# Optimization experiments

Hardware: AMD Instinct MI355X
Metric: run time of the kernel (lower is better)

The kernel has to match this reference:

```python
import jax, jax.numpy as jnp
import numpy as np

# dims
T, B, IN, OUT = 100, 128, 512, 512
# LIF constants (match torch defaults / init_kwargs)
TAU_TRACE, TAU_MEM, TAU_SYN, DT = 20.0, 20.0, 5.0, 1.0
THRESH, SSB = 1.0, 0.03


def setup_inputs() -> dict:
    key = jax.random.key(0)
    k1, k2 = jax.random.split(key)
    input_spikes = (jax.random.uniform(k1, (T, B, IN)) < 0.1).astype(jnp.float32)
    W = jax.random.normal(k2, (OUT, IN), dtype=jnp.float32) * (1.0 / IN ** 0.5)
    return {"input_spikes": input_spikes, "W": W}


def reference(input_spikes, W):
    alpha = jnp.exp(jnp.asarray(-DT / TAU_SYN, jnp.float32))   # synaptic decay
    beta = jnp.exp(jnp.asarray(-DT / TAU_MEM, jnp.float32))    # membrane decay
    gamma = jnp.exp(jnp.asarray(-DT / TAU_TRACE, jnp.float32)) # trace decay
    Tn, Bn, _ = input_spikes.shape
    out_f, in_f = W.shape
    I0 = jnp.zeros((Bn, out_f), jnp.float32)
    U0 = jnp.zeros((Bn, out_f), jnp.float32)
    tr0 = jnp.zeros((Bn, out_f, in_f), jnp.float32)

    def step(carry, x_t):
        I, U, trace = carry
        I = alpha * I + x_t @ W.T                      # (B, out)
        U = beta * U + I
        S = (U >= THRESH).astype(jnp.float32)
        U_pre = U                                      # first U_hist append (pre-reset)
        U = U - S * THRESH                             # reset
        du = jnp.abs(U - THRESH)
        sigma_prime = 1.0 / (1.0 + SSB * du) ** 2      # SuperSpike surrogate
        # eligibility trace: outer product of surrogate grad and input spikes
        trace = gamma * trace + sigma_prime[:, :, None] * x_t[:, None, :]
        U_post = U                                     # second U_hist append (post-reset)
        U = U - S * THRESH                             # second subtraction (as in source)
        return (I, U, trace), (S, U_pre, U_post)

    (_, _, trace), (S, U_pre, U_post) = jax.lax.scan(step, (I0, U0, tr0), input_spikes)
    # interleave pre/post membrane snapshots -> (2T, B, out), matching the torch stack order
    U_hist = jnp.stack([U_pre, U_post], axis=1).reshape(2 * Tn, Bn, out_f)
    return S, U_hist, trace
```

## Files before the change

kernel.cpp:

```cpp
#include <hip/hip_runtime.h>

#define T_STEPS 100
#define B_N     128
#define IN_F    512
#define OUT_F   512

#define ALPHA_D 0.8187307530779818
#define BETA_D  0.9512294245007140

typedef __attribute__((ext_vector_type(8))) short bf16x8;
typedef __attribute__((ext_vector_type(4))) float f32x4;

static __device__ __forceinline__ unsigned short f2bf(float f) {
    union { float f; unsigned int u; } v; v.f = f;
    unsigned int r = (v.u + 0x7FFFu + ((v.u >> 16) & 1u)) >> 16;
    return (unsigned short)r;
}

__global__ __launch_bounds__(256) void transposeW(const float* __restrict__ W,
                                                  float* __restrict__ Wt) {
    __shared__ float tile[32][33];
    const int bx = blockIdx.x & 15;
    const int by = blockIdx.x >> 4;
    const int tx = threadIdx.x & 31;
    const int ty = threadIdx.x >> 5;
#pragma unroll
    for (int k = 0; k < 32; k += 8) {
        int o = by * 32 + ty + k;
        tile[ty + k][tx] = W[o * IN_F + bx * 32 + tx];
    }
    __syncthreads();
#pragma unroll
    for (int k = 0; k < 32; k += 8) {
        int i = bx * 32 + ty + k;
        Wt[i * OUT_F + by * 32 + tx] = tile[tx][ty + k];
    }
}

__global__ __launch_bounds__(256) void syn_current(const float* __restrict__ x,
                                                   const float* __restrict__ Wt,
                                                   double* __restrict__ C) {
    const int tb  = blockIdx.x;
    const int tid = threadIdx.x;

    __shared__ int s_idx[IN_F];
    __shared__ int s_cnt;

    if (tid < 64) {
        const float* xr = x + (size_t)tb * IN_F;
        int base = 0;
#pragma unroll
        for (int j = 0; j < 8; ++j) {
            const float v = xr[j * 64 + tid];
            const unsigned long long m = __ballot(v > 0.5f);
            if (v > 0.5f) {
                const int pos = base + __popcll(m & ((1ull << tid) - 1ull));
                s_idx[pos] = j * 64 + tid;
            }
            base += __popcll(m);
        }
        if (tid == 0) s_cnt = base;
    }
    __syncthreads();

    const int cnt = s_cnt;
    double c0 = 0.0, c1 = 0.0;
    const float* W0 = Wt + tid;
    const float* W1 = Wt + tid + 256;
    for (int k = 0; k < cnt; ++k) {
        const int i = s_idx[k];
        c0 += (double)W0[(size_t)i * OUT_F];
        c1 += (double)W1[(size_t)i * OUT_F];
    }

    double* Cr = C + (size_t)tb * OUT_F;
    Cr[tid]       = c0;
    Cr[tid + 256] = c1;
}

#define LIF_STEP(BUF, J, CB)                                                   \
    {                                                                          \
        const int t = (CB) * 10 + (J);                                         \
        I = ALPHA_D * I + BUF[J];                                              \
        U = BETA_D * U + I;                                                    \
        const double Sv = (U >= 1.0) ? 1.0 : 0.0;                              \
        S_out[(size_t)t * N + pos] = (float)Sv;                                \
        Uh[(size_t)(2 * t) * N + pos] = (float)U;                              \
        U -= Sv;                                                               \
        Uh[(size_t)(2 * t + 1) * N + pos] = (float)U;                          \
        U -= Sv;                                                               \
    }

__global__ __launch_bounds__(256) void lif_pointwise(const double* __restrict__ C,
                                                     float* __restrict__ S_out,
                                                     float* __restrict__ Uh) {
    const int pos = blockIdx.x * 256 + threadIdx.x;
    const size_t N = (size_t)B_N * OUT_F;

    double I = 0.0, U = 0.0;
    double bufA[10], bufB[10];

#pragma unroll
    for (int j = 0; j < 10; ++j) bufA[j] = C[(size_t)j * N + pos];

    for (int cb = 0; cb < 10; cb += 2) {
#pragma unroll
        for (int j = 0; j < 10; ++j) bufB[j] = C[((size_t)(cb + 1) * 10 + j) * N + pos];
#pragma unroll
        for (int j = 0; j < 10; ++j) LIF_STEP(bufA, j, cb)
        if (cb + 2 < 10) {
#pragma unroll
            for (int j = 0; j < 10; ++j) bufA[j] = C[((size_t)(cb + 2) * 10 + j) * N + pos];
        }
#pragma unroll
        for (int j = 0; j < 10; ++j) LIF_STEP(bufB, j, cb + 1)
    }
}

__global__ __launch_bounds__(256) void trace_mfma(const float* __restrict__ x,
                                                  const float* __restrict__ Uh,
                                                  float* __restrict__ trace) {
    __shared__ unsigned short Pa[128 * 128];
    __shared__ unsigned short Xb[128 * 128];

    const int idx  = blockIdx.x;
    const int xcd  = idx & 7;
    const int slot = idx >> 3;
    const int b    = xcd * 16 + (slot >> 4);
    const int tile = slot & 15;
    const int ot   = tile >> 2;
    const int it   = tile & 3;
    const int tid  = threadIdx.x;

    char* const pbase = (char*)Pa;
    char* const xbase = (char*)Xb;

#pragma unroll
    for (int r = 0; r < 8; ++r) {
        const int g  = tid + r * 256;
        const int i  = g & 127;
        const int kg = g >> 7;
        unsigned int h[4];
#pragma unroll
        for (int jj = 0; jj < 4; ++jj) {
            const int t0 = kg * 8 + jj * 2, t1 = t0 + 1;
            float v0 = 0.f, v1 = 0.f;
            if (t0 < T_STEPS) v0 = x[(size_t)t0 * (B_N * IN_F) + b * IN_F + it * 128 + i];
            if (t1 < T_STEPS) v1 = x[(size_t)t1 * (B_N * IN_F) + b * IN_F + it * 128 + i];
            h[jj] = (unsigned int)f2bf(v0) | ((unsigned int)f2bf(v1) << 16);
        }
        unsigned int off = (unsigned int)(i * 256 + kg * 16) ^ ((unsigned int)(i & 7) << 4);
        *(uint4*)(xbase + off) = make_uint4(h[0], h[1], h[2], h[3]);
    }

#pragma unroll
    for (int r = 0; r < 8; ++r) {
        const int g  = tid + r * 256;
        const int o  = g & 127;
        const int kg = g >> 7;
        unsigned int h[4];
#pragma unroll
        for (int jj = 0; jj < 4; ++jj) {
            unsigned int hw[2];
#pragma unroll
            for (int e = 0; e < 2; ++e) {
                const int t = kg * 8 + jj * 2 + e;
                float p = 0.f;
                if (t < T_STEPS) {
                    const float u  = Uh[(size_t)(2 * t + 1) * (B_N * OUT_F) + b * OUT_F + ot * 128 + o];
                    const float du = fabsf(u - 1.0f);
                    const float d  = 1.0f + 0.03f * du;
                    const float gp = __expf(-0.05f * (float)(T_STEPS - 1 - t));
                    p = gp / (d * d);
                }
                hw[e] = f2bf(p);
            }
            h[jj] = hw[0] | (hw[1] << 16);
        }
        unsigned int off = (unsigned int)(o * 256 + kg * 16) ^ ((unsigned int)(o & 7) << 4);
        *(uint4*)(pbase + off) = make_uint4(h[0], h[1], h[2], h[3]);
    }
    __syncthreads();

    const int w    = tid >> 6;
    const int l    = tid & 63;
    const int wo   = (w >> 1) * 64;
    const int wi   = (w & 1) * 64;
    const int lo16 = l & 15;
    const int g4   = l >> 4;

    f32x4 acc[4][4];
#pragma unroll
    for (int m = 0; m < 4; ++m)
#pragma unroll
        for (int n = 0; n < 4; ++n) acc[m][n] = (f32x4){0.f, 0.f, 0.f, 0.f};

#pragma unroll
    for (int kk = 0; kk < 4; ++kk) {
        bf16x8 af[4], bfr[4];
#pragma unroll
        for (int m = 0; m < 4; ++m) {
            const int row = wo + m * 16 + lo16;
            const unsigned int off = (unsigned int)(row * 256 + kk * 64 + g4 * 16)
                                     ^ ((unsigned int)(row & 7) << 4);
            af[m] = *(const bf16x8*)(pbase + off);
        }
#pragma unroll
        for (int n = 0; n < 4; ++n) {
            const int row = wi + n * 16 + lo16;
            const unsigned int off = (unsigned int)(row * 256 + kk * 64 + g4 * 16)
                                     ^ ((unsigned int)(row & 7) << 4);
            bfr[n] = *(const bf16x8*)(xbase + off);
        }
#pragma unroll
        for (int m = 0; m < 4; ++m)
#pragma unroll
            for (int n = 0; n < 4; ++n)
                acc[m][n] = __builtin_amdgcn_mfma_f32_16x16x32_bf16(af[m], bfr[n], acc[m][n], 0, 0, 0);
    }

    float* tb = trace + (size_t)b * (OUT_F * IN_F);
#pragma unroll
    for (int m = 0; m < 4; ++m) {
#pragma unroll
        for (int rr = 0; rr < 4; ++rr) {
            const int o = ot * 128 + wo + m * 16 + g4 * 4 + rr;
#pragma unroll
            for (int n = 0; n < 4; ++n) {
                const int i = it * 128 + wi + n * 16 + lo16;
                tb[(size_t)o * IN_F + i] = acc[m][n][rr];
            }
        }
    }
}

extern "C" void kernel_launch(void* const* d_in, const int* in_sizes, int n_in,
                              void* d_out, int out_size, void* d_ws, size_t ws_size,
                              hipStream_t stream) {
    const float* x = (const float*)d_in[0];
    const float* W = (const float*)d_in[1];

    float* out   = (float*)d_out;
    float* S_out = out;
    float* Uh    = out + (size_t)T_STEPS * B_N * OUT_F;
    float* trace = Uh + (size_t)2 * T_STEPS * B_N * OUT_F;

    float* Wt = (float*)d_ws;

    double* C = (double*)trace;

    transposeW<<<256, 256, 0, stream>>>(W, Wt);
    syn_current<<<T_STEPS * B_N, 256, 0, stream>>>(x, Wt, C);
    lif_pointwise<<<B_N * OUT_F / 256, 256, 0, stream>>>(C, S_out, Uh);
    trace_mfma<<<16 * B_N, 256, 0, stream>>>(x, Uh, trace);
}
```

Before: 158.1 us.

## Precompute bf16 surrogate and input operands in workspace for trace MFMA

Adds a kernel that converts the input spikes to a padded bf16 K-major layout, and has the LIF kernel emit the decay-weighted surrogate gradient directly as packed bf16. The trace MFMA kernel then loads both operands with contiguous 16-byte vector loads instead of gathering strided fp32 values and converting them per tile. This removes redundant conversion and scattered loads across the 16 tiles per batch. In exchange it adds an extra kernel launch, extra workspace traffic and per-step exp/division work in the LIF kernel. It falls back to the old path when the workspace is too small.

```diff
diff --git a/kernel.cpp b/kernel.cpp
--- a/kernel.cpp
+++ b/kernel.cpp
@@ -4,6 +4,7 @@
 #define B_N     128
 #define IN_F    512
 #define OUT_F   512
+#define KPAD    128
 
 #define ALPHA_D 0.8187307530779818
 #define BETA_D  0.9512294245007140
@@ -11,10 +12,9 @@
 typedef __attribute__((ext_vector_type(8))) short bf16x8;
 typedef __attribute__((ext_vector_type(4))) float f32x4;
 
-static __device__ __forceinline__ unsigned short f2bf(float f) {
+static __device__ __forceinline__ unsigned int f2bf(float f) {
     union { float f; unsigned int u; } v; v.f = f;
-    unsigned int r = (v.u + 0x7FFFu + ((v.u >> 16) & 1u)) >> 16;
-    return (unsigned short)r;
+    return (v.u + 0x7FFFu + ((v.u >> 16) & 1u)) >> 16;
 }
 
 __global__ __launch_bounds__(256) void transposeW(const float* __restrict__ W,
@@ -34,6 +34,31 @@
     for (int k = 0; k < 32; k += 8) {
         int i = bx * 32 + ty + k;
         Wt[i * OUT_F + by * 32 + tx] = tile[tx][ty + k];
+    }
+}
+
+__global__ __launch_bounds__(256) void x_to_bf16(const float* __restrict__ x,
+                                                 unsigned short* __restrict__ Xbf) {
+    const int b   = blockIdx.x & (B_N - 1);
+    const int i0  = (blockIdx.x >> 7) * 128;
+    const int tid = threadIdx.x;
+
+#pragma unroll
+    for (int r = 0; r < 8; ++r) {
+        const int g = tid + r * 256;
+        const int i = i0 + (g & 127);
+        const int c = g >> 7;
+        unsigned int h[4];
+#pragma unroll
+        for (int jj = 0; jj < 4; ++jj) {
+            const int t0 = c * 8 + jj * 2, t1 = t0 + 1;
+            float v0 = 0.f, v1 = 0.f;
+            if (t0 < T_STEPS) v0 = x[(size_t)t0 * (B_N * IN_F) + b * IN_F + i];
+            if (t1 < T_STEPS) v1 = x[(size_t)t1 * (B_N * IN_F) + b * IN_F + i];
+            h[jj] = f2bf(v0) | (f2bf(v1) << 16);
+        }
+        *(uint4*)((char*)Xbf + (size_t)(b * IN_F + i) * (KPAD * 2) + c * 16) =
+            make_uint4(h[0], h[1], h[2], h[3]);
     }
 }
 
@@ -88,17 +113,27 @@
         Uh[(size_t)(2 * t) * N + pos] = (float)U;                              \
         U -= Sv;                                                               \
         Uh[(size_t)(2 * t + 1) * N + pos] = (float)U;                          \
+        if (Pq) {                                                              \
+            const float du = fabsf((float)U - 1.0f);                           \
+            const float dd = 1.0f + 0.03f * du;                                \
+            const float pv = __expf(-0.05f * (float)(T_STEPS - 1 - t)) / (dd * dd); \
+            const unsigned int hw = f2bf(pv);                                  \
+            if ((J) & 1) Pq[(size_t)pos * 64 + (t >> 1)] = plo | (hw << 16);   \
+            else plo = hw;                                                     \
+        }                                                                      \
         U -= Sv;                                                               \
     }
 
 __global__ __launch_bounds__(256) void lif_pointwise(const double* __restrict__ C,
                                                      float* __restrict__ S_out,
-                                                     float* __restrict__ Uh) {
+                                                     float* __restrict__ Uh,
+                                                     unsigned int* __restrict__ Pq) {
     const int pos = blockIdx.x * 256 + threadIdx.x;
     const size_t N = (size_t)B_N * OUT_F;
 
     double I = 0.0, U = 0.0;
     double bufA[10], bufB[10];
+    unsigned int plo = 0;
 
 #pragma unroll
     for (int j = 0; j < 10; ++j) bufA[j] = C[(size_t)j * N + pos];
@@ -115,11 +150,16 @@
 #pragma unroll
         for (int j = 0; j < 10; ++j) LIF_STEP(bufB, j, cb + 1)
     }
-}
-
-__global__ __launch_bounds__(256) void trace_mfma(const float* __restrict__ x,
-                                                  const float* __restrict__ Uh,
-                                                  float* __restrict__ trace) {
+
+    if (Pq) {
+#pragma unroll
+        for (int k = 0; k < 14; ++k) Pq[(size_t)pos * 64 + 50 + k] = 0u;
+    }
+}
+
+__global__ __launch_bounds__(256) void trace_mfma_pre(const unsigned short* __restrict__ Pbf,
+                                                      const unsigned short* __restrict__ Xbf,
+                                                      float* __restrict__ trace) {
     __shared__ unsigned short Pa[128 * 128];
     __shared__ unsigned short Xb[128 * 128];
 
@@ -134,6 +174,91 @@
 
     char* const pbase = (char*)Pa;
     char* const xbase = (char*)Xb;
+    const char* const Pg = (const char*)Pbf + (size_t)(b * OUT_F + ot * 128) * (KPAD * 2);
+    const char* const Xg = (const char*)Xbf + (size_t)(b * IN_F + it * 128) * (KPAD * 2);
+
+#pragma unroll
+    for (int r = 0; r < 8; ++r) {
+        const int chunk = tid + r * 256;
+        const int row   = chunk >> 4;
+        const int c     = chunk & 15;
+        const unsigned int loff = (unsigned int)(row * 256) + ((unsigned int)(c * 16) ^ ((unsigned int)(row & 7) << 4));
+        const uint4 vp = *(const uint4*)(Pg + (size_t)row * 256 + c * 16);
+        const uint4 vx = *(const uint4*)(Xg + (size_t)row * 256 + c * 16);
+        *(uint4*)(pbase + loff) = vp;
+        *(uint4*)(xbase + loff) = vx;
+    }
+    __syncthreads();
+
+    const int w    = tid >> 6;
+    const int l    = tid & 63;
+    const int wo   = (w >> 1) * 64;
+    const int wi   = (w & 1) * 64;
+    const int lo16 = l & 15;
+    const int g4   = l >> 4;
+
+    f32x4 acc[4][4];
+#pragma unroll
+    for (int m = 0; m < 4; ++m)
+#pragma unroll
+        for (int n = 0; n < 4; ++n) acc[m][n] = (f32x4){0.f, 0.f, 0.f, 0.f};
+
+#pragma unroll
+    for (int kk = 0; kk < 4; ++kk) {
+        bf16x8 af[4], bfr[4];
+#pragma unroll
+        for (int m = 0; m < 4; ++m) {
+            const int row = wo + m * 16 + lo16;
+            const unsigned int off = (unsigned int)(row * 256 + kk * 64 + g4 * 16)
+                                     ^ ((unsigned int)(row & 7) << 4);
+            af[m] = *(const bf16x8*)(pbase + off);
+        }
+#pragma unroll
+        for (int n = 0; n < 4; ++n) {
+            const int row = wi + n * 16 + lo16;
+            const unsigned int off = (unsigned int)(row * 256 + kk * 64 + g4 * 16)
+                                     ^ ((unsigned int)(row & 7) << 4);
+            bfr[n] = *(const bf16x8*)(xbase + off);
+        }
+#pragma unroll
+        for (int m = 0; m < 4; ++m)
+#pragma unroll
+            for (int n = 0; n < 4; ++n)
+                acc[m][n] = __builtin_amdgcn_mfma_f32_16x16x32_bf16(af[m], bfr[n], acc[m][n], 0, 0, 0);
+    }
+
+    float* tb = trace + (size_t)b * (OUT_F * IN_F);
+#pragma unroll
+    for (int m = 0; m < 4; ++m) {
+#pragma unroll
+        for (int rr = 0; rr < 4; ++rr) {
+            const int o = ot * 128 + wo + m * 16 + g4 * 4 + rr;
+#pragma unroll
+            for (int n = 0; n < 4; ++n) {
+                const int i = it * 128 + wi + n * 16 + lo16;
+                tb[(size_t)o * IN_F + i] = acc[m][n][rr];
+            }
+        }
+    }
+}
+
+__global__ __launch_bounds__(256) void trace_mfma(const float* __restrict__ x,
+                                                  const float* __restrict__ Uh,
+                                                  float* __restrict__ trace) {
+    __shared__ unsigned short Pa[128 * 128];
+    __shared__ unsigned short Xb[128 * 128];
+
+    const int idx  = blockIdx.x;
+    const int xcd  = idx & 7;
+    const int slot = idx >> 3;
+    const int b    = xcd * 16 + (slot >> 4);
+    const int tile = slot & 15;
+    const int ot   = tile >> 2;
+    const int it   = tile & 3;
+    const int tid  = threadIdx.x;
+
+    char* const pbase = (char*)Pa;
+    char* const xbase = (char*)Xb;
 
 #pragma unroll
     for (int r = 0; r < 8; ++r) {
@@ -147,7 +272,7 @@
             float v0 = 0.f, v1 = 0.f;
             if (t0 < T_STEPS) v0 = x[(size_t)t0 * (B_N * IN_F) + b * IN_F + it * 128 + i];
             if (t1 < T_STEPS) v1 = x[(size_t)t1 * (B_N * IN_F) + b * IN_F + it * 128 + i];
-            h[jj] = (unsigned int)f2bf(v0) | ((unsigned int)f2bf(v1) << 16);
+            h[jj] = f2bf(v0) | (f2bf(v1) << 16);
         }
         unsigned int off = (unsigned int)(i * 256 + kg * 16) ^ ((unsigned int)(i & 7) << 4);
         *(uint4*)(xbase + off) = make_uint4(h[0], h[1], h[2], h[3]);
@@ -245,12 +370,23 @@
     float* Uh    = out + (size_t)T_STEPS * B_N * OUT_F;
     float* trace = Uh + (size_t)2 * T_STEPS * B_N * OUT_F;
 
-    float* Wt = (float*)d_ws;
+    const size_t WT_BYTES = (size_t)IN_F * OUT_F * 4;
+    const size_t BF_BYTES = (size_t)B_N * 512 * KPAD * 2;
+    const bool   ws_ok    = ws_size >= WT_BYTES + 2 * BF_BYTES;
+
+    float*          Wt  = (float*)d_ws;
+    unsigned short* Xbf = (unsigned short*)((char*)d_ws + WT_BYTES);
+    unsigned short* Pbf = (unsigned short*)((char*)d_ws + WT_BYTES + BF_BYTES);
 
     double* C = (double*)trace;
 
     transposeW<<<256, 256, 0, stream>>>(W, Wt);
+    if (ws_ok) x_to_bf16<<<512, 256, 0, stream>>>(x, Xbf);
     syn_current<<<T_STEPS * B_N, 256, 0, stream>>>(x, Wt, C);
-    lif_pointwise<<<B_N * OUT_F / 256, 256, 0, stream>>>(C, S_out, Uh);
-    trace_mfma<<<16 * B_N, 256, 0, stream>>>(x, Uh, trace);
-}
+    lif_pointwise<<<B_N * OUT_F / 256, 256, 0, stream>>>(C, S_out, Uh,
+                                                         ws_ok ? (unsigned int*)Pbf : nullptr);
+    if (ws_ok)
+        trace_mfma_pre<<<16 * B_N, 256, 0, stream>>>(Pbf, Xbf, trace);
+    else
+        trace_mfma<<<16 * B_N, 256, 0, stream>>>(x, Uh, trace);
+}
```

Result: slower. 165.3 us (+4.6%).

## Fuse synaptic current, LIF recurrence and trace MFMA into one kernel

Applied to the files above, without the earlier changes.

Replaces the three-kernel pipeline (syn_current, lif_pointwise, trace_mfma) with a spike-index prep kernel plus one fused kernel per (batch, 256-output) block. That kernel computes the sparse current, runs the LIF recurrence and keeps the surrogate weights in LDS for the trace matmul. This avoids the double-precision current buffer round trip and the re-read of Uh. The catch is that only 256 blocks are launched, each running a serial 100-step recurrence followed by a long trace phase, so occupancy is low. It also needs extra workspace and keeps the old path as a fallback.

```diff
diff --git a/kernel.cpp b/kernel.cpp
--- a/kernel.cpp
+++ b/kernel.cpp
@@ -11,10 +11,9 @@
 typedef __attribute__((ext_vector_type(8))) short bf16x8;
 typedef __attribute__((ext_vector_type(4))) float f32x4;
 
-static __device__ __forceinline__ unsigned short f2bf(float f) {
+static __device__ __forceinline__ unsigned int f2bf(float f) {
     union { float f; unsigned int u; } v; v.f = f;
-    unsigned int r = (v.u + 0x7FFFu + ((v.u >> 16) & 1u)) >> 16;
-    return (unsigned short)r;
+    return (v.u + 0x7FFFu + ((v.u >> 16) & 1u)) >> 16;
 }
 
 __global__ __launch_bounds__(256) void transposeW(const float* __restrict__ W,
@@ -34,6 +33,181 @@
     for (int k = 0; k < 32; k += 8) {
         int i = bx * 32 + ty + k;
         Wt[i * OUT_F + by * 32 + tx] = tile[tx][ty + k];
+    }
+}
+
+__global__ __launch_bounds__(256) void prep_lists(const float* __restrict__ x,
+                                                  unsigned char* __restrict__ Lg,
+                                                  int* __restrict__ Cg) {
+    const int pair = blockIdx.x * 4 + (threadIdx.x >> 6);
+    const int lane = threadIdx.x & 63;
+    const int t = pair >> 7, b = pair & 127;
+    const float* xr = x + (size_t)pair * IN_F;
+    unsigned char* lrow = Lg + (size_t)b * (128 * 128) + t * 128;
+    int base = 0, clo = 0;
+#pragma unroll
+    for (int j = 0; j < 8; ++j) {
+        const float v = xr[j * 64 + lane];
+        const unsigned long long m = __ballot(v > 0.5f);
+        if (v > 0.5f) {
+            const int pos = base + __popcll(m & ((1ull << lane) - 1ull));
+            lrow[pos] = (unsigned char)((j * 64 + lane) & 255);
+        }
+        base += __popcll(m);
+        if (j == 3) clo = base;
+    }
+    if (lane == 0) Cg[b * 128 + t] = clo | (base << 16);
+}
+
+__global__ __launch_bounds__(256) void fused_lif_trace(const float* __restrict__ x,
+                                                       const float* __restrict__ Wt,
+                                                       const unsigned char* __restrict__ Lg,
+                                                       const int* __restrict__ Cg,
+                                                       float* __restrict__ S_out,
+                                                       float* __restrict__ Uh,
+                                                       float* __restrict__ trace) {
+    __shared__ char smem[98816];
+    char* const Psm = smem;
+    char* const Lsm = smem + 65536;
+    int*  const Csm = (int*)(smem + 81920);
+    char* const Xsm = smem + 82432;
+
+    const int tid = threadIdx.x;
+    const int b   = blockIdx.x & 127;
+    const int ob  = blockIdx.x >> 7;
+
+    {
+        const uint4 z = make_uint4(0u, 0u, 0u, 0u);
+#pragma unroll
+        for (int r = 0; r < 16; ++r) ((uint4*)Psm)[tid + r * 256] = z;
+        const uint4* Lg4 = (const uint4*)(Lg + (size_t)b * (128 * 128));
+#pragma unroll
+        for (int r = 0; r < 4; ++r) ((uint4*)Lsm)[tid + r * 256] = Lg4[tid + r * 256];
+        if (tid < 128) Csm[tid] = Cg[b * 128 + tid];
+    }
+    __syncthreads();
+
+    {
+        const int og = ob * 256 + tid;
+        const float* const Wlo = Wt + og;
+        const float* const Whi = Wt + (size_t)256 * OUT_F + og;
+        const size_t N = (size_t)B_N * OUT_F;
+        const size_t base = (size_t)b * OUT_F + og;
+        double I = 0.0, U = 0.0;
+        for (int t = 0; t < T_STEPS; ++t) {
+            const int cp   = Csm[t];
+            const int clo  = cp & 0xFFFF;
+            const int ctot = cp >> 16;
+            const unsigned char* lp = (const unsigned char*)Lsm + t * 128;
+
+            double c0 = 0.0, c1 = 0.0, c2 = 0.0, c3 = 0.0;
+            int k = 0;
+            for (; k + 3 < clo; k += 4) {
+                c0 += (double)Wlo[(size_t)lp[k]     * OUT_F];
+                c1 += (double)Wlo[(size_t)lp[k + 1] * OUT_F];
+                c2 += (double)Wlo[(size_t)lp[k + 2] * OUT_F];
+                c3 += (double)Wlo[(size_t)lp[k + 3] * OUT_F];
+            }
+            for (; k < clo; ++k) c0 += (double)Wlo[(size_t)lp[k] * OUT_F];
+            for (; k + 3 < ctot; k += 4) {
+                c0 += (double)Whi[(size_t)lp[k]     * OUT_F];
+                c1 += (double)Whi[(size_t)lp[k + 1] * OUT_F];
+                c2 += (double)Whi[(size_t)lp[k + 2] * OUT_F];
+                c3 += (double)Whi[(size_t)lp[k + 3] * OUT_F];
+            }
+            for (; k < ctot; ++k) c0 += (double)Whi[(size_t)lp[k] * OUT_F];
+            const double c = (c0 + c2) + (c1 + c3);
+
+            I = ALPHA_D * I + c;
+            U = BETA_D * U + I;
+            const double Sv = (U >= 1.0) ? 1.0 : 0.0;
+            __builtin_nontemporal_store((float)Sv, S_out + (size_t)t * N + base);
+            __builtin_nontemporal_store((float)U,  Uh + (size_t)(2 * t) * N + base);
+            U -= Sv;
+            __builtin_nontemporal_store((float)U,  Uh + (size_t)(2 * t + 1) * N + base);
+            {
+                const float du = fabsf((float)U - 1.0f);
+                const float dd = 1.0f + 0.03f * du;
+                const float pv = __expf(-0.05f * (float)(T_STEPS - 1 - t)) / (dd * dd);
+                *(unsigned short*)(Psm + (((unsigned)(tid * 256 + 2 * t)) ^
+                                          (((unsigned)(tid & 7)) << 4))) = (unsigned short)f2bf(pv);
+            }
+            U -= Sv;
+        }
+    }
+    __syncthreads();
+
+    const int w = tid >> 6, l = tid & 63, lo16 = l & 15, g4 = l >> 4;
+
+    bf16x8 af[4][4];
+#pragma unroll
+    for (int m = 0; m < 4; ++m) {
+        const int row = w * 64 + m * 16 + lo16;
+#pragma unroll
+        for (int kk = 0; kk < 4; ++kk) {
+            const unsigned off = (unsigned)(row * 256 + kk * 64 + g4 * 16)
+                                 ^ ((unsigned)(row & 7) << 4);
+            af[m][kk] = *(const bf16x8*)(Psm + off);
+        }
+    }
+
+    float* const tb = trace + (size_t)b * (OUT_F * IN_F);
+
+    for (int it = 0; it < 8; ++it) {
+#pragma unroll
+        for (int r = 0; r < 4; ++r) {
+            const int g  = tid + r * 256;
+            const int i  = g & 63;
+            const int kg = g >> 6;
+            unsigned int h[4];
+#pragma unroll
+            for (int jj = 0; jj < 4; ++jj) {
+                const int t0 = kg * 8 + jj * 2, t1 = t0 + 1;
+                float v0 = 0.f, v1 = 0.f;
+                if (t0 < T_STEPS) v0 = x[(size_t)t0 * (B_N * IN_F) + b * IN_F + it * 64 + i];
+                if (t1 < T_STEPS) v1 = x[(size_t)t1 * (B_N * IN_F) + b * IN_F + it * 64 + i];
+                h[jj] = f2bf(v0) | (f2bf(v1) << 16);
+            }
+            const unsigned loff = (unsigned)(i * 256) +
+                (((unsigned)(kg * 16)) ^ (((unsigned)(i & 7)) << 4));
+            *(uint4*)(Xsm + loff) = make_uint4(h[0], h[1], h[2], h[3]);
+        }
+        __syncthreads();
+
+        f32x4 acc[4][4];
+#pragma unroll
+        for (int m = 0; m < 4; ++m)
+#pragma unroll
+            for (int n = 0; n < 4; ++n) acc[m][n] = (f32x4){0.f, 0.f, 0.f, 0.f};
+
+#pragma unroll
+        for (int kk = 0; kk < 4; ++kk) {
+            bf16x8 bfr[4];
+#pragma unroll
+            for (int n = 0; n < 4; ++n) {
+                const int row = n * 16 + lo16;
+                const unsigned off = (unsigned)(row * 256 + kk * 64 + g4 * 16)
+                                     ^ ((unsigned)(row & 7) << 4);
+                bfr[n] = *(const bf16x8*)(Xsm + off);
+            }
+#pragma unroll
+            for (int m = 0; m < 4; ++m)
+#pragma unroll
+                for (int n = 0; n < 4; ++n)
+                    acc[m][n] = __builtin_amdgcn_mfma_f32_16x16x32_bf16(af[m][kk], bfr[n], acc[m][n], 0, 0, 0);
+        }
+
+#pragma unroll
+        for (int m = 0; m < 4; ++m)
+#pragma unroll
+            for (int rr = 0; rr < 4; ++rr) {
+                const int o = ob * 256 + w * 64 + m * 16 + g4 * 4 + rr;
+#pragma unroll
+                for (int n = 0; n < 4; ++n)
+                    __builtin_nontemporal_store(acc[m][n][rr],
+                        tb + (size_t)o * IN_F + it * 64 + n * 16 + lo16);
+            }
+        __syncthreads();
     }
 }
 
@@ -147,7 +321,7 @@
             float v0 = 0.f, v1 = 0.f;
             if (t0 < T_STEPS) v0 = x[(size_t)t0 * (B_N * IN_F) + b * IN_F + it * 128 + i];
             if (t1 < T_STEPS) v1 = x[(size_t)t1 * (B_N * IN_F) + b * IN_F + it * 128 + i];
-            h[jj] = (unsigned int)f2bf(v0) | ((unsigned int)f2bf(v1) << 16);
+            h[jj] = f2bf(v0) | (f2bf(v1) << 16);
         }
         unsigned int off = (unsigned int)(i * 256 + kg * 16) ^ ((unsigned int)(i & 7) << 4);
         *(uint4*)(xbase + off) = make_uint4(h[0], h[1], h[2], h[3]);
@@ -245,12 +419,23 @@
     float* Uh    = out + (size_t)T_STEPS * B_N * OUT_F;
     float* trace = Uh + (size_t)2 * T_STEPS * B_N * OUT_F;
 
-    float* Wt = (float*)d_ws;
-
-    double* C = (double*)trace;
+    const size_t WT_BYTES = (size_t)IN_F * OUT_F * 4;
+    const size_t L_BYTES  = (size_t)128 * 128 * 128;
+    const size_t C_BYTES  = (size_t)128 * 128 * 4;
+    const bool   ws_ok    = ws_size >= WT_BYTES + L_BYTES + C_BYTES;
+
+    float*         Wt = (float*)d_ws;
+    unsigned char* Lg = (unsigned char*)d_ws + WT_BYTES;
+    int*           Cg = (int*)((char*)d_ws + WT_BYTES + L_BYTES);
 
     transposeW<<<256, 256, 0, stream>>>(W, Wt);
-    syn_current<<<T_STEPS * B_N, 256, 0, stream>>>(x, Wt, C);
-    lif_pointwise<<<B_N * OUT_F / 256, 256, 0, stream>>>(C, S_out, Uh);
-    trace_mfma<<<16 * B_N, 256, 0, stream>>>(x, Uh, trace);
-}
+    if (ws_ok) {
+        prep_lists<<<3200, 256, 0, stream>>>(x, Lg, Cg);
+        fused_lif_trace<<<256, 256, 0, stream>>>(x, Wt, Lg, Cg, S_out, Uh, trace);
+    } else {
+        double* C = (double*)trace;
+        syn_current<<<T_STEPS * B_N, 256, 0, stream>>>(x, Wt, C);
+        lif_pointwise<<<B_N * OUT_F / 256, 256, 0, stream>>>(C, S_out, Uh);
+        trace_mfma<<<16 * B_N, 256, 0, stream>>>(x, Uh, trace);
+    }
+}
```

After: 297.1 us. 1.88x slower.

## Pack input spikes into bitmasks and tile trace MFMA over input columns

Applied to the files above, without the earlier changes.

Adds a prologue in the synaptic-current kernel that packs each (b,i) spike time series into 128-bit bitmasks. The trace kernel then unpacks these bits straight into bf16 operands instead of re-reading fp32 spikes from global memory. The trace kernel is also restructured: each block now covers 64 output rows for one batch and loops over 8 input-column tiles. The surrogate operand stays resident in registers across that loop, and results are written with nontemporal stores. This cuts input traffic and redundant surrogate computation, at the cost of extra barriers per tile and a smaller grid.

```diff
diff --git a/kernel.cpp b/kernel.cpp
--- a/kernel.cpp
+++ b/kernel.cpp
@@ -11,10 +11,9 @@
 typedef __attribute__((ext_vector_type(8))) short bf16x8;
 typedef __attribute__((ext_vector_type(4))) float f32x4;
 
-static __device__ __forceinline__ unsigned short f2bf(float f) {
+static __device__ __forceinline__ unsigned int f2bf(float f) {
     union { float f; unsigned int u; } v; v.f = f;
-    unsigned int r = (v.u + 0x7FFFu + ((v.u >> 16) & 1u)) >> 16;
-    return (unsigned short)r;
+    return (v.u + 0x7FFFu + ((v.u >> 16) & 1u)) >> 16;
 }
 
 __global__ __launch_bounds__(256) void transposeW(const float* __restrict__ W,
@@ -37,11 +36,39 @@
     }
 }
 
-__global__ __launch_bounds__(256) void syn_current(const float* __restrict__ x,
-                                                   const float* __restrict__ Wt,
-                                                   double* __restrict__ C) {
-    const int tb  = blockIdx.x;
+__global__ __launch_bounds__(256) void syn_plus(const float* __restrict__ x,
+                                                const float* __restrict__ Wt,
+                                                double* __restrict__ C,
+                                                unsigned int* __restrict__ Xbits) {
     const int tid = threadIdx.x;
+
+    if ((int)blockIdx.x < 512) {
+        const int b    = blockIdx.x >> 2;
+        const int q    = blockIdx.x & 3;
+        const int half = tid >> 7;
+        const int i    = q * 128 + (tid & 127);
+        const float* xc = x + (size_t)b * IN_F + i;
+        unsigned int wA = 0u, wB = 0u;
+        if (half == 0) {
+#pragma unroll
+            for (int tt = 0; tt < 32; ++tt)
+                wA |= (xc[(size_t)tt * (B_N * IN_F)] > 0.5f ? 1u : 0u) << tt;
+#pragma unroll
+            for (int tt = 0; tt < 32; ++tt)
+                wB |= (xc[(size_t)(32 + tt) * (B_N * IN_F)] > 0.5f ? 1u : 0u) << tt;
+        } else {
+#pragma unroll
+            for (int tt = 0; tt < 32; ++tt)
+                wA |= (xc[(size_t)(64 + tt) * (B_N * IN_F)] > 0.5f ? 1u : 0u) << tt;
+#pragma unroll
+            for (int tt = 0; tt < 4; ++tt)
+                wB |= (xc[(size_t)(96 + tt) * (B_N * IN_F)] > 0.5f ? 1u : 0u) << tt;
+        }
+        ((uint2*)Xbits)[(size_t)(b * IN_F + i) * 2 + half] = make_uint2(wA, wB);
+        return;
+    }
+
+    const int tb = (int)blockIdx.x - 512;
 
     __shared__ int s_idx[IN_F];
     __shared__ int s_cnt;
@@ -117,119 +144,113 @@
     }
 }
 
-__global__ __launch_bounds__(256) void trace_mfma(const float* __restrict__ x,
-                                                  const float* __restrict__ Uh,
+__global__ __launch_bounds__(256) void trace_bits(const float* __restrict__ Uh,
+                                                  const unsigned int* __restrict__ Xbits,
                                                   float* __restrict__ trace) {
-    __shared__ unsigned short Pa[128 * 128];
-    __shared__ unsigned short Xb[128 * 128];
-
-    const int idx  = blockIdx.x;
-    const int xcd  = idx & 7;
-    const int slot = idx >> 3;
-    const int b    = xcd * 16 + (slot >> 4);
-    const int tile = slot & 15;
-    const int ot   = tile >> 2;
-    const int it   = tile & 3;
-    const int tid  = threadIdx.x;
-
-    char* const pbase = (char*)Pa;
-    char* const xbase = (char*)Xb;
-
-#pragma unroll
-    for (int r = 0; r < 8; ++r) {
-        const int g  = tid + r * 256;
-        const int i  = g & 127;
-        const int kg = g >> 7;
-        unsigned int h[4];
-#pragma unroll
-        for (int jj = 0; jj < 4; ++jj) {
-            const int t0 = kg * 8 + jj * 2, t1 = t0 + 1;
-            float v0 = 0.f, v1 = 0.f;
-            if (t0 < T_STEPS) v0 = x[(size_t)t0 * (B_N * IN_F) + b * IN_F + it * 128 + i];
-            if (t1 < T_STEPS) v1 = x[(size_t)t1 * (B_N * IN_F) + b * IN_F + it * 128 + i];
-            h[jj] = (unsigned int)f2bf(v0) | ((unsigned int)f2bf(v1) << 16);
-        }
-        unsigned int off = (unsigned int)(i * 256 + kg * 16) ^ ((unsigned int)(i & 7) << 4);
-        *(uint4*)(xbase + off) = make_uint4(h[0], h[1], h[2], h[3]);
-    }
-
-#pragma unroll
-    for (int r = 0; r < 8; ++r) {
-        const int g  = tid + r * 256;
-        const int o  = g & 127;
-        const int kg = g >> 7;
-        unsigned int h[4];
-#pragma unroll
-        for (int jj = 0; jj < 4; ++jj) {
-            unsigned int hw[2];
-#pragma unroll
-            for (int e = 0; e < 2; ++e) {
-                const int t = kg * 8 + jj * 2 + e;
-                float p = 0.f;
-                if (t < T_STEPS) {
-                    const float u  = Uh[(size_t)(2 * t + 1) * (B_N * OUT_F) + b * OUT_F + ot * 128 + o];
-                    const float du = fabsf(u - 1.0f);
-                    const float d  = 1.0f + 0.03f * du;
-                    const float gp = __expf(-0.05f * (float)(T_STEPS - 1 - t));
-                    p = gp / (d * d);
+    __shared__ char Psm[16384];
+    __shared__ char Xsm[16384];
+
+    const int tid = threadIdx.x;
+    const int b   = blockIdx.x & 127;
+    const int ot  = blockIdx.x >> 7;
+
+    {
+        const int o_l = tid & 63;
+        const int cg  = tid >> 6;
+        const float* up = Uh + (size_t)b * OUT_F + ot * 64 + o_l;
+#pragma unroll
+        for (int cc = 0; cc < 4; ++cc) {
+            const int c = cg * 4 + cc;
+            unsigned int h[4];
+#pragma unroll
+            for (int jj = 0; jj < 4; ++jj) {
+                unsigned int hw[2];
+#pragma unroll
+                for (int e = 0; e < 2; ++e) {
+                    const int t = c * 8 + jj * 2 + e;
+                    float p = 0.f;
+                    if (t < T_STEPS) {
+                        const float u  = up[(size_t)(2 * t + 1) * (B_N * OUT_F)];
+                        const float du = fabsf(u - 1.0f);
+                        const float dd = 1.0f + 0.03f * du;
+                        p = __expf(-0.05f * (float)(T_STEPS - 1 - t)) / (dd * dd);
+                    }
+                    hw[e] = f2bf(p);
                 }
-                hw[e] = f2bf(p);
-            }
-            h[jj] = hw[0] | (hw[1] << 16);
-        }
-        unsigned int off = (unsigned int)(o * 256 + kg * 16) ^ ((unsigned int)(o & 7) << 4);
-        *(uint4*)(pbase + off) = make_uint4(h[0], h[1], h[2], h[3]);
+                h[jj] = hw[0] | (hw[1] << 16);
+            }
+            const unsigned loff = (unsigned)(o_l * 256) +
+                (((unsigned)(c * 16)) ^ (((unsigned)(o_l & 7)) << 4));
+            *(uint4*)(Psm + loff) = make_uint4(h[0], h[1], h[2], h[3]);
+        }
     }
     __syncthreads();
 
-    const int w    = tid >> 6;
-    const int l    = tid & 63;
-    const int wo   = (w >> 1) * 64;
-    const int wi   = (w & 1) * 64;
-    const int lo16 = l & 15;
-    const int g4   = l >> 4;
-
-    f32x4 acc[4][4];
-#pragma unroll
-    for (int m = 0; m < 4; ++m)
-#pragma unroll
-        for (int n = 0; n < 4; ++n) acc[m][n] = (f32x4){0.f, 0.f, 0.f, 0.f};
-
-#pragma unroll
-    for (int kk = 0; kk < 4; ++kk) {
-        bf16x8 af[4], bfr[4];
-#pragma unroll
-        for (int m = 0; m < 4; ++m) {
-            const int row = wo + m * 16 + lo16;
-            const unsigned int off = (unsigned int)(row * 256 + kk * 64 + g4 * 16)
-                                     ^ ((unsigned int)(row & 7) << 4);
-            af[m] = *(const bf16x8*)(pbase + off);
-        }
-#pragma unroll
-        for (int n = 0; n < 4; ++n) {
-            const int row = wi + n * 16 + lo16;
-            const unsigned int off = (unsigned int)(row * 256 + kk * 64 + g4 * 16)
-                                     ^ ((unsigned int)(row & 7) << 4);
-            bfr[n] = *(const bf16x8*)(xbase + off);
-        }
-#pragma unroll
-        for (int m = 0; m < 4; ++m)
+    const int w = tid >> 6, l = tid & 63, lo16 = l & 15, g4 = l >> 4;
+    bf16x8 af[4];
+    {
+        const int row = w * 16 + lo16;
+#pragma unroll
+        for (int kk = 0; kk < 4; ++kk) {
+            const unsigned off = (unsigned)(row * 256 + kk * 64 + g4 * 16)
+                                 ^ ((unsigned)(row & 7) << 4);
+            af[kk] = *(const bf16x8*)(Psm + off);
+        }
+    }
+
+    float* const tb = trace + (size_t)b * (OUT_F * IN_F) + (size_t)(ot * 64) * IN_F;
+    const int i_l  = tid & 63;
+    const int wsel = tid >> 6;
+
+    for (int it = 0; it < 8; ++it) {
+        __syncthreads();
+
+        {
+            const unsigned int word =
+                Xbits[(size_t)(b * IN_F + it * 64 + i_l) * 4 + wsel];
+#pragma unroll
+            for (int j = 0; j < 4; ++j) {
+                unsigned int h[4];
+#pragma unroll
+                for (int m = 0; m < 4; ++m) {
+                    const unsigned b0 = (word >> (j * 8 + 2 * m)) & 1u;
+                    const unsigned b1 = (word >> (j * 8 + 2 * m + 1)) & 1u;
+                    h[m] = b0 * 0x3F80u | b1 * 0x3F800000u;
+                }
+                const int c = wsel * 4 + j;
+                const unsigned loff = (unsigned)(i_l * 256) +
+                    (((unsigned)(c * 16)) ^ (((unsigned)(i_l & 7)) << 4));
+                *(uint4*)(Xsm + loff) = make_uint4(h[0], h[1], h[2], h[3]);
+            }
+        }
+        __syncthreads();
+
+        f32x4 acc[4];
+#pragma unroll
+        for (int n = 0; n < 4; ++n) acc[n] = (f32x4){0.f, 0.f, 0.f, 0.f};
+
+#pragma unroll
+        for (int kk = 0; kk < 4; ++kk) {
+            bf16x8 bfr[4];
+#pragma unroll
+            for (int n = 0; n < 4; ++n) {
+                const int row = n * 16 + lo16;
+                const unsigned off = (unsigned)(row * 256 + kk * 64 + g4 * 16)
+                                     ^ ((unsigned)(row & 7) << 4);
+                bfr[n] = *(const bf16x8*)(Xsm + off);
+            }
 #pragma unroll
             for (int n = 0; n < 4; ++n)
-                acc[m][n] = __builtin_amdgcn_mfma_f32_16x16x32_bf16(af[m], bfr[n], acc[m][n], 0, 0, 0);
-    }
-
-    float* tb = trace + (size_t)b * (OUT_F * IN_F);
-#pragma unroll
-    for (int m = 0; m < 4; ++m) {
+                acc[n] = __builtin_amdgcn_mfma_f32_16x16x32_bf16(af[kk], bfr[n], acc[n], 0, 0, 0);
+        }
+
 #pragma unroll
         for (int rr = 0; rr < 4; ++rr) {
-            const int o = ot * 128 + wo + m * 16 + g4 * 4 + rr;
-#pragma unroll
-            for (int n = 0; n < 4; ++n) {
-                const int i = it * 128 + wi + n * 16 + lo16;
-                tb[(size_t)o * IN_F + i] = acc[m][n][rr];
-            }
+            const int o = w * 16 + g4 * 4 + rr;
+#pragma unroll
+            for (int n = 0; n < 4; ++n)
+                __builtin_nontemporal_store(acc[n][rr],
+                    tb + (size_t)o * IN_F + it * 64 + n * 16 + lo16);
         }
     }
 }
@@ -245,12 +266,13 @@
     float* Uh    = out + (size_t)T_STEPS * B_N * OUT_F;
     float* trace = Uh + (size_t)2 * T_STEPS * B_N * OUT_F;
 
-    float* Wt = (float*)d_ws;
+    float*        Wt    = (float*)d_ws;
+    unsigned int* Xbits = (unsigned int*)((char*)d_ws + (size_t)IN_F * OUT_F * 4);
 
     double* C = (double*)trace;
 
     transposeW<<<256, 256, 0, stream>>>(W, Wt);
-    syn_current<<<T_STEPS * B_N, 256, 0, stream>>>(x, Wt, C);
+    syn_plus<<<512 + T_STEPS * B_N, 256, 0, stream>>>(x, Wt, C, Xbits);
     lif_pointwise<<<B_N * OUT_F / 256, 256, 0, stream>>>(C, S_out, Uh);
-    trace_mfma<<<16 * B_N, 256, 0, stream>>>(x, Uh, trace);
-}
+    trace_bits<<<1024, 256, 0, stream>>>(Uh, Xbits, trace);
+}
```

New measurement: 147.6 us. -6.6%, faster.
